# Kernel tuning notes

Measured on AMD Instinct MI355X. Metric: run time of the kernel, lower is better.

## Reference

```python
import jax, jax.numpy as jnp
import numpy as np

B, T, W, F, H = 4, 1024, 33, 512, 8
DK = F // H


def setup_inputs() -> dict:
    key = jax.random.key(0)
    ks = jax.random.split(key, 12)
    s = 1.0 / np.sqrt(F)
    return {
        "query": jax.random.normal(ks[0], (B, T, F), jnp.float32),
        "key": jax.random.normal(ks[1], (B, T, W, F), jnp.float32),
        "value": jax.random.normal(ks[2], (B, T, W, F), jnp.float32),
        "mask": jnp.ones((B, 1, T, W), jnp.int32),
        "Wq": jax.random.uniform(ks[3], (F, F), jnp.float32, -s, s),
        "bq": jax.random.uniform(ks[4], (F,), jnp.float32, -s, s),
        "Wk": jax.random.uniform(ks[5], (F, F), jnp.float32, -s, s),
        "bk": jax.random.uniform(ks[6], (F,), jnp.float32, -s, s),
        "Wv": jax.random.uniform(ks[7], (F, F), jnp.float32, -s, s),
        "bv": jax.random.uniform(ks[8], (F,), jnp.float32, -s, s),
        "Wo": jax.random.uniform(ks[9], (F, F), jnp.float32, -s, s),
        "bo": jax.random.uniform(ks[10], (F,), jnp.float32, -s, s),
    }


def reference(query, key, value, mask, Wq, bq, Wk, bk, Wv, bv, Wo, bo):
    b, t, w, f = key.shape
    # projections
    q = (query @ Wq + bq).reshape(b, t, H, DK)            # (B,T,H,Dk)
    k = (key @ Wk + bk).reshape(b, t, w, H, DK)           # (B,T,W,H,Dk)
    v = (value @ Wv + bv).reshape(b, t, w, H, DK)
    # windowed scores: each query attends to its own window of keys
    scores = jnp.einsum("bthd,btwhd->bhtw", q, k) / jnp.sqrt(jnp.asarray(DK, q.dtype))
    m = (mask == 0)                                       # (B,1,T,W), broadcasts over heads
    min_value = jnp.finfo(scores.dtype).min
    scores = jnp.where(m, min_value, scores)
    attn = jax.nn.softmax(scores, axis=-1)
    attn = jnp.where(m, 0.0, attn)                        # (B,H,T,W)
    x = jnp.einsum("bhtw,btwhd->bthd", attn, v).reshape(b, t, H * DK)
    return x @ Wo + bo
```

## Files before the change

### kernel.cpp

```cpp
#include <hip/hip_runtime.h>
#include <hip/hip_bf16.h>
#include <cstdint>

#define B_ 4
#define T_ 1024
#define W_ 33
#define F_ 512
#define H_ 8
#define DK_ 64

typedef __attribute__((ext_vector_type(8))) short short8;
typedef __attribute__((ext_vector_type(4))) float f32x4;

__device__ __forceinline__ float b2f(ushort u) {
  return __uint_as_float(((uint32_t)u) << 16);
}
__device__ __forceinline__ ushort f2b(float f) {
  union { __hip_bfloat16 b; ushort u; } cv;
  cv.b = __float2bfloat16(f);
  return cv.u;
}

__global__ void convert_w(const float* __restrict__ Wq, const float* __restrict__ Wk,
                          const float* __restrict__ Wv, const float* __restrict__ Wo,
                          ushort* __restrict__ out)
{
  int which = blockIdx.y;
  const float* src = (which == 0) ? Wq : (which == 1) ? Wk : (which == 2) ? Wv : Wo;
  ushort* dst = out + (size_t)which * 262144;
  int idx = blockIdx.x * 256 + threadIdx.x;
  int e = idx & 7;
  int l = (idx >> 3) & 63;
  float v;
  if (which == 1) {
    int kc  = (idx >> 9) & 1;
    int ntf = (idx >> 10) & 31;
    int h   = idx >> 15;
    v = src[(size_t)(ntf * 16 + (l & 15)) * 512 + h * 64 + kc * 32 + ((l >> 4) << 3) + e];
  } else {
    int kc = (idx >> 9) & 15;
    int nt = idx >> 13;
    int k = kc * 32 + ((l >> 4) << 3) + e;
    int n = (nt << 4) + (l & 15);
    v = src[(size_t)k * 512 + n];
  }
  dst[idx] = f2b(v);
}

template<bool A_F32, bool OUT_F32>
__global__ __launch_bounds__(256, 2)
void gemm_pipe(const void* __restrict__ Ap, const ushort* __restrict__ Bf,
               const float* __restrict__ bias, void* __restrict__ Cp, float scale)
{
  __shared__ ushort lA[3][128 * 64];

  const int tid  = threadIdx.x;
  const int lane = tid & 63;
  const int wid  = tid >> 6;
  const int wr   = wid >> 1, wc = wid & 1;
  const int lrow = lane & 15;
  const int lk8  = (lane >> 4) * 8;

  int nwg  = gridDim.x;
  int xcd  = blockIdx.x & 7;
  int slot = blockIdx.x >> 3;
  int q8   = nwg >> 3, r8 = nwg & 7;
  int base = (xcd < r8) ? xcd * (q8 + 1) : r8 * (q8 + 1) + (xcd - r8) * q8;
  int L    = base + slot;
  int bm   = L >> 2;
  int bn   = L & 3;

  int lb_[4];
  size_t asrc_[4];
#pragma unroll
  for (int p = 0; p < 4; ++p) {
    int c   = p * 256 + tid;
    int row = c >> 3;
    int kc  = (c & 7) * 8;
    lb_[p]  = (row * 128 + kc * 2) ^ ((row & 7) << 4);
    asrc_[p] = (size_t)(bm * 128 + row) * 512 + kc;
  }

  const int ntb = bn * 8 + wc * 4;

  float4 P0a0[4], P0a1[4], P1a0[4], P1a1[4];
  short8 P0r[4], P1r[4];
  short8 Q0[8], Q1[8];

  auto issueA = [&](int ks, float4 (&d0)[4], float4 (&d1)[4], short8 (&dr)[4]) {
#pragma unroll
    for (int p = 0; p < 4; ++p) {
      if (A_F32) {
        const float* src = (const float*)Ap + asrc_[p] + ks * 64;
        d0[p] = *(const float4*)src;
        d1[p] = *(const float4*)(src + 4);
      } else {
        dr[p] = *(const short8*)((const ushort*)Ap + asrc_[p] + ks * 64);
      }
    }
  };
  auto lwriteA = [&](int buf, float4 (&d0)[4], float4 (&d1)[4], short8 (&dr)[4]) {
#pragma unroll
    for (int p = 0; p < 4; ++p) {
      short8 hv;
      if (A_F32) {
        hv[0] = (short)f2b(d0[p].x); hv[1] = (short)f2b(d0[p].y);
        hv[2] = (short)f2b(d0[p].z); hv[3] = (short)f2b(d0[p].w);
        hv[4] = (short)f2b(d1[p].x); hv[5] = (short)f2b(d1[p].y);
        hv[6] = (short)f2b(d1[p].z); hv[7] = (short)f2b(d1[p].w);
      } else {
        hv = dr[p];
      }
      *(short8*)((char*)lA[buf] + lb_[p]) = hv;
    }
  };
  auto loadB = [&](int ks, short8 (&dq)[8]) {
#pragma unroll
    for (int kk = 0; kk < 2; ++kk)
#pragma unroll
      for (int nf = 0; nf < 4; ++nf)
        dq[kk * 4 + nf] = *(const short8*)(Bf +
            (((size_t)(ntb + nf) * 16 + ks * 2 + kk) * 64 + lane) * 8);
  };

  f32x4 acc[4][4];
#pragma unroll
  for (int i = 0; i < 4; ++i)
#pragma unroll
    for (int j = 0; j < 4; ++j) acc[i][j] = {0.f, 0.f, 0.f, 0.f};

  auto computeStep = [&](int buf, short8 (&dq)[8]) {
#pragma unroll
    for (int kk = 0; kk < 2; ++kk) {
      short8 af[4];
#pragma unroll
      for (int mf = 0; mf < 4; ++mf) {
        int row = wr * 64 + mf * 16 + lrow;
        int off = (row * 128 + (kk * 32 + lk8) * 2) ^ ((row & 7) << 4);
        af[mf] = *(const short8*)((const char*)lA[buf] + off);
      }
#pragma unroll
      for (int mf = 0; mf < 4; ++mf)
#pragma unroll
        for (int nf = 0; nf < 4; ++nf)
          acc[mf][nf] = __builtin_amdgcn_mfma_f32_16x16x32_bf16(af[mf], dq[kk * 4 + nf], acc[mf][nf], 0, 0, 0);
    }
  };

  issueA(0, P0a0, P0a1, P0r);
  issueA(1, P1a0, P1a1, P1r);
  loadB(0, Q0);
  lwriteA(0, P0a0, P0a1, P0r);
  __syncthreads();

#define GSTEP(T, PWa0, PWa1, PWr, PIa0, PIa1, PIr, QW, QR)                    \
  {                                                                           \
    if ((T) + 1 < 8) lwriteA(((T) + 1) % 3, PWa0, PWa1, PWr);                 \
    if ((T) + 2 < 8) issueA((T) + 2, PIa0, PIa1, PIr);                        \
    if ((T) + 1 < 8) loadB((T) + 1, QW);                                      \
    computeStep((T) % 3, QR);                                                 \
    if ((T) < 7) __syncthreads();                                             \
  }

  GSTEP(0, P1a0, P1a1, P1r, P0a0, P0a1, P0r, Q1, Q0)
  GSTEP(1, P0a0, P0a1, P0r, P1a0, P1a1, P1r, Q0, Q1)
  GSTEP(2, P1a0, P1a1, P1r, P0a0, P0a1, P0r, Q1, Q0)
  GSTEP(3, P0a0, P0a1, P0r, P1a0, P1a1, P1r, Q0, Q1)
  GSTEP(4, P1a0, P1a1, P1r, P0a0, P0a1, P0r, Q1, Q0)
  GSTEP(5, P0a0, P0a1, P0r, P1a0, P1a1, P1r, Q0, Q1)
  GSTEP(6, P1a0, P1a1, P1r, P0a0, P0a1, P0r, Q1, Q0)
  GSTEP(7, P0a0, P0a1, P0r, P1a0, P1a1, P1r, Q0, Q1)
#undef GSTEP

  float bs[4];
#pragma unroll
  for (int nf = 0; nf < 4; ++nf)
    bs[nf] = bias[bn * 128 + wc * 64 + nf * 16 + lrow];

  const int r0 = (lane >> 4) * 4;
#pragma unroll
  for (int mf = 0; mf < 4; ++mf) {
#pragma unroll
    for (int nf = 0; nf < 4; ++nf) {
      int gcol = bn * 128 + wc * 64 + nf * 16 + lrow;
#pragma unroll
      for (int r = 0; r < 4; ++r) {
        int grow = bm * 128 + wr * 64 + mf * 16 + r0 + r;
        float val = (acc[mf][nf][r] + bs[nf]) * scale;
        if (OUT_F32) ((float*)Cp)[(size_t)grow * 512 + gcol] = val;
        else         ((ushort*)Cp)[(size_t)grow * 512 + gcol] = f2b(val);
      }
    }
  }
}

__global__ __launch_bounds__(256, 4)
void r_gemm(const ushort* __restrict__ q, const ushort* __restrict__ WkR,
            ushort* __restrict__ R)
{
  const int tid  = threadIdx.x;
  const int lane = tid & 63;
  const int wid  = tid >> 6;
  const int lr   = lane & 15;
  const int l8   = (lane >> 4) * 8;
  const int mg   = blockIdx.x >> 1;
  const int nh   = blockIdx.x & 1;
  const int h    = blockIdx.y;
  const int m0   = mg * 64;
  const int ntb  = nh * 16 + wid * 4;

  short8 af[2][4], bg[2][4];
#pragma unroll
  for (int ks = 0; ks < 2; ++ks)
#pragma unroll
    for (int mf = 0; mf < 4; ++mf)
      af[ks][mf] = *(const short8*)(q + (size_t)(m0 + mf * 16 + lr) * 512 + h * 64 + ks * 32 + l8);
#pragma unroll
  for (int ks = 0; ks < 2; ++ks)
#pragma unroll
    for (int nf = 0; nf < 4; ++nf)
      bg[ks][nf] = *(const short8*)(WkR + ((size_t)((h * 32 + ntb + nf) * 2 + ks) * 64 + lane) * 8);

  f32x4 acc[4][4];
#pragma unroll
  for (int i = 0; i < 4; ++i)
#pragma unroll
    for (int j = 0; j < 4; ++j) acc[i][j] = {0.f, 0.f, 0.f, 0.f};

#pragma unroll
  for (int ks = 0; ks < 2; ++ks)
#pragma unroll
    for (int mf = 0; mf < 4; ++mf)
#pragma unroll
      for (int nf = 0; nf < 4; ++nf)
        acc[mf][nf] = __builtin_amdgcn_mfma_f32_16x16x32_bf16(af[ks][mf], bg[ks][nf], acc[mf][nf], 0, 0, 0);

  const int rr = (lane >> 4) * 4;
#pragma unroll
  for (int mf = 0; mf < 4; ++mf)
#pragma unroll
    for (int nf = 0; nf < 4; ++nf) {
      int col = nh * 256 + wid * 64 + nf * 16 + lr;
#pragma unroll
      for (int r = 0; r < 4; ++r) {
        int row = m0 + mf * 16 + rr + r;
        R[((size_t)row * 8 + h) * 512 + col] = f2b(acc[mf][nf][r]);
      }
    }
}

__global__ __launch_bounds__(256, 3)
void attn_fused(const float* __restrict__ key, const float* __restrict__ value,
                const ushort* __restrict__ R, const int* __restrict__ mask,
                ushort* __restrict__ g, float* __restrict__ asum)
{
  __shared__ float sc[H_][W_ + 3];
  __shared__ float lin[H_];
  __shared__ int   msk[W_];

  const int tid  = threadIdx.x;
  const int lane = tid & 63;
  const int wv   = tid >> 6;
  const int bt   = blockIdx.x;

  if (tid < W_) msk[tid] = mask[(size_t)bt * W_ + tid];

  float Rf[8][8];
  {
    const ushort* Rb = R + (size_t)bt * 4096 + lane * 8;
#pragma unroll
    for (int h = 0; h < 8; ++h) {
      short8 rv = *(const short8*)(Rb + h * 512);
#pragma unroll
      for (int j = 0; j < 8; ++j) Rf[h][j] = b2f((ushort)rv[j]);
    }
  }

  const float* kb = key + (size_t)bt * (W_ * 512) + lane * 8;
  for (int w = wv; w < W_; w += 4) {
    float4 k0 = *(const float4*)(kb + (size_t)w * 512);
    float4 k1 = *(const float4*)(kb + (size_t)w * 512 + 4);
    float s[8];
#pragma unroll
    for (int h = 0; h < 8; ++h)
      s[h] = k0.x * Rf[h][0] + k0.y * Rf[h][1] + k0.z * Rf[h][2] + k0.w * Rf[h][3]
           + k1.x * Rf[h][4] + k1.y * Rf[h][5] + k1.z * Rf[h][6] + k1.w * Rf[h][7];
#pragma unroll
    for (int m = 1; m < 64; m <<= 1)
#pragma unroll
      for (int h = 0; h < 8; ++h) s[h] += __shfl_xor(s[h], m, 64);
    if (lane == 0) {
#pragma unroll
      for (int h = 0; h < 8; ++h) sc[h][w] = s[h];
    }
  }
  __syncthreads();

  if (tid < H_) {
    float mx = -3.4028234663852886e38f;
    bool any = false;
    for (int w = 0; w < W_; ++w)
      if (msk[w]) { mx = fmaxf(mx, sc[tid][w]); any = true; }
    float ss = 0.f;
    for (int w = 0; w < W_; ++w) {
      float e = msk[w] ? __expf(sc[tid][w] - mx) : 0.f;
      sc[tid][w] = e;
      ss += e;
    }
    lin[tid] = any ? 1.f / ss : 0.f;
    asum[(size_t)bt * H_ + tid] = any ? 1.f : 0.f;
  }
  __syncthreads();

  const float* vb2 = value + (size_t)bt * (W_ * 512) + tid * 2;
  float g0[8], g1[8];
#pragma unroll
  for (int h = 0; h < 8; ++h) { g0[h] = 0.f; g1[h] = 0.f; }

#pragma unroll
  for (int w = 0; w < W_; ++w) {
    float2 v = *(const float2*)(vb2 + (size_t)w * 512);
#pragma unroll
    for (int h = 0; h < 8; ++h) {
      float a = sc[h][w];
      g0[h] += a * v.x;
      g1[h] += a * v.y;
    }
  }

  ushort* gb = g + (size_t)bt * 4096 + tid * 2;
#pragma unroll
  for (int h = 0; h < 8; ++h) {
    float inv = lin[h];
    ushort2 pk;
    pk.x = f2b(g0[h] * inv);
    pk.y = f2b(g1[h] * inv);
    *(ushort2*)(gb + h * 512) = pk;
  }
}

__global__ __launch_bounds__(256, 2)
void x_proj(const ushort* __restrict__ g, const ushort* __restrict__ WtV,
            const float* __restrict__ bv, const float* __restrict__ asum,
            ushort* __restrict__ x)
{
  const int tid  = threadIdx.x;
  const int lane = tid & 63;
  const int wid  = tid >> 6;
  const int lr   = lane & 15;
  const int l8   = (lane >> 4) * 8;
  const int h    = blockIdx.y;
  const int m0   = blockIdx.x * 256 + wid * 64;
  const int ntb  = h * 4;

  f32x4 acc[4][4];
#pragma unroll
  for (int i = 0; i < 4; ++i)
#pragma unroll
    for (int j = 0; j < 4; ++j) acc[i][j] = {0.f, 0.f, 0.f, 0.f};

  short8 a0[4], a1[4], b0[4], b1[4];

  auto issue = [&](int ks, short8 (&A)[4], short8 (&Bq)[4]) {
#pragma unroll
    for (int mf = 0; mf < 4; ++mf)
      A[mf] = *(const short8*)(g + ((size_t)(m0 + mf * 16 + lr) * 8 + h) * 512 + ks * 32 + l8);
#pragma unroll
    for (int nf = 0; nf < 4; ++nf)
      Bq[nf] = *(const short8*)(WtV + ((size_t)((ntb + nf) * 16 + ks) * 64 + lane) * 8);
  };
  auto step = [&](short8 (&A)[4], short8 (&Bq)[4]) {
#pragma unroll
    for (int mf = 0; mf < 4; ++mf)
#pragma unroll
      for (int nf = 0; nf < 4; ++nf)
        acc[mf][nf] = __builtin_amdgcn_mfma_f32_16x16x32_bf16(A[mf], Bq[nf], acc[mf][nf], 0, 0, 0);
  };

  issue(0, a0, b0);
  issue(1, a1, b1);
#pragma unroll 1
  for (int ks = 0; ks < 16; ks += 2) {
    step(a0, b0);
    if (ks + 2 < 16) issue(ks + 2, a0, b0);
    step(a1, b1);
    if (ks + 3 < 16) issue(ks + 3, a1, b1);
  }

  float bvv[4];
#pragma unroll
  for (int nf = 0; nf < 4; ++nf)
    bvv[nf] = bv[h * 64 + nf * 16 + lr];

  const int rr = (lane >> 4) * 4;
#pragma unroll
  for (int mf = 0; mf < 4; ++mf)
#pragma unroll
    for (int nf = 0; nf < 4; ++nf) {
      int col = h * 64 + nf * 16 + lr;
#pragma unroll
      for (int r = 0; r < 4; ++r) {
        int row = m0 + mf * 16 + rr + r;
        float val = acc[mf][nf][r] + asum[(size_t)row * 8 + h] * bvv[nf];
        x[(size_t)row * 512 + col] = f2b(val);
      }
    }
}

extern "C" void kernel_launch(void* const* d_in, const int* in_sizes, int n_in,
                              void* d_out, int out_size, void* d_ws, size_t ws_size,
                              hipStream_t stream)
{
  const float* query = (const float*)d_in[0];
  const float* key   = (const float*)d_in[1];
  const float* value = (const float*)d_in[2];
  const int*   mask  = (const int*)d_in[3];
  const float* Wq    = (const float*)d_in[4];
  const float* bq    = (const float*)d_in[5];
  const float* Wk    = (const float*)d_in[6];
  const float* bk    = (const float*)d_in[7];
  const float* Wv    = (const float*)d_in[8];
  const float* bv    = (const float*)d_in[9];
  const float* Wo    = (const float*)d_in[10];
  const float* bo    = (const float*)d_in[11];
  (void)bk;

  char* ws = (char*)d_ws;
  ushort* Wt   = (ushort*)ws;
  ushort* WtQ  = Wt;
  ushort* WkR  = Wt + 262144;
  ushort* WtV  = Wt + 524288;
  ushort* WtO  = Wt + 786432;
  ushort* qws  = (ushort*)(ws + (size_t)2  * 1024 * 1024);
  ushort* Rws  = (ushort*)(ws + (size_t)6  * 1024 * 1024);
  ushort* gws  = (ushort*)(ws + (size_t)38 * 1024 * 1024);
  float*  asum = (float*) (ws + (size_t)70 * 1024 * 1024);
  ushort* xws  = (ushort*)(ws + (size_t)71 * 1024 * 1024);

  convert_w<<<dim3(1024, 4), 256, 0, stream>>>(Wq, Wk, Wv, Wo, Wt);

  gemm_pipe<true, false><<<dim3(128, 1), 256, 0, stream>>>(query, WtQ, bq, qws, 0.125f);

  r_gemm<<<dim3(128, 8), 256, 0, stream>>>(qws, WkR, Rws);

  attn_fused<<<dim3(B_ * T_, 1), 256, 0, stream>>>(key, value, Rws, mask, gws, asum);

  x_proj<<<dim3(16, 8), 256, 0, stream>>>(gws, WtV, bv, asum, xws);

  gemm_pipe<false, true><<<dim3(128, 1), 256, 0, stream>>>(xws, WtO, bo, d_out, 1.0f);
}
```

Measured before the change: 193.3 us.

## Assign one wavefront per query position in windowed attention kernel

Each wavefront now handles one (b,t) position instead of one block per position. This removes block-wide __syncthreads and the serial 8-thread softmax. The score reduction uses a transpose-style select-and-shuffle so each lane ends up holding one head's sum. The mask is kept as a ballot bitmask, and value accumulation uses 8 columns per lane across all heads with wide bf16 stores. The cost is many more registers per thread (64 accumulators plus 64 R values), which may lower occupancy, and each wave now streams all 33 key and value rows serially.

```diff
diff --git a/kernel.cpp b/kernel.cpp
--- a/kernel.cpp
+++ b/kernel.cpp
@@ -249,21 +249,22 @@
     }
 }
 
-__global__ __launch_bounds__(256, 3)
+__global__ __launch_bounds__(256)
 void attn_fused(const float* __restrict__ key, const float* __restrict__ value,
                 const ushort* __restrict__ R, const int* __restrict__ mask,
                 ushort* __restrict__ g, float* __restrict__ asum)
 {
-  __shared__ float sc[H_][W_ + 3];
-  __shared__ float lin[H_];
-  __shared__ int   msk[W_];
+  __shared__ float lsc[4][8][36];
+  __shared__ float linv[4][8];
 
   const int tid  = threadIdx.x;
   const int lane = tid & 63;
   const int wv   = tid >> 6;
-  const int bt   = blockIdx.x;
-
-  if (tid < W_) msk[tid] = mask[(size_t)bt * W_ + tid];
+  const int bt   = blockIdx.x * 4 + wv;
+
+  int mreg = 0;
+  if (lane < W_) mreg = mask[(size_t)bt * W_ + lane];
+  unsigned long long mbits = __ballot(mreg != 0);
 
   float Rf[8][8];
   {
@@ -277,7 +278,8 @@
   }
 
   const float* kb = key + (size_t)bt * (W_ * 512) + lane * 8;
-  for (int w = wv; w < W_; w += 4) {
+#pragma unroll 2
+  for (int w = 0; w < W_; ++w) {
     float4 k0 = *(const float4*)(kb + (size_t)w * 512);
     float4 k1 = *(const float4*)(kb + (size_t)w * 512 + 4);
     float s[8];
@@ -286,56 +288,69 @@
       s[h] = k0.x * Rf[h][0] + k0.y * Rf[h][1] + k0.z * Rf[h][2] + k0.w * Rf[h][3]
            + k1.x * Rf[h][4] + k1.y * Rf[h][5] + k1.z * Rf[h][6] + k1.w * Rf[h][7];
 #pragma unroll
-    for (int m = 1; m < 64; m <<= 1)
+    for (int m = 1; m <= 4; m <<= 1)
 #pragma unroll
       for (int h = 0; h < 8; ++h) s[h] += __shfl_xor(s[h], m, 64);
-    if (lane == 0) {
-#pragma unroll
-      for (int h = 0; h < 8; ++h) sc[h][w] = s[h];
-    }
-  }
-  __syncthreads();
-
-  if (tid < H_) {
-    float mx = -3.4028234663852886e38f;
-    bool any = false;
-    for (int w = 0; w < W_; ++w)
-      if (msk[w]) { mx = fmaxf(mx, sc[tid][w]); any = true; }
-    float ss = 0.f;
-    for (int w = 0; w < W_; ++w) {
-      float e = msk[w] ? __expf(sc[tid][w] - mx) : 0.f;
-      sc[tid][w] = e;
-      ss += e;
-    }
-    lin[tid] = any ? 1.f / ss : 0.f;
-    asum[(size_t)bt * H_ + tid] = any ? 1.f : 0.f;
-  }
-  __syncthreads();
-
-  const float* vb2 = value + (size_t)bt * (W_ * 512) + tid * 2;
-  float g0[8], g1[8];
-#pragma unroll
-  for (int h = 0; h < 8; ++h) { g0[h] = 0.f; g1[h] = 0.f; }
-
-#pragma unroll
+    float ta = (lane & 1) ? s[1] : s[0];
+    float tb = (lane & 1) ? s[3] : s[2];
+    float tc = (lane & 1) ? s[5] : s[4];
+    float td = (lane & 1) ? s[7] : s[6];
+    float ua = (lane & 2) ? tb : ta;
+    float ub = (lane & 2) ? td : tc;
+    float t  = (lane & 4) ? ub : ua;
+    t += __shfl_xor(t, 8, 64);
+    t += __shfl_xor(t, 16, 64);
+    t += __shfl_xor(t, 32, 64);
+    t = ((mbits >> w) & 1ull) ? t : -3.0e38f;
+    if (lane < 8) lsc[wv][lane][w] = t;
+  }
+
+  const int hh = lane & 7;
+  float mx = -3.4028234663852886e38f;
+  for (int w = 0; w < W_; ++w) mx = fmaxf(mx, lsc[wv][hh][w]);
+  float ss = 0.f;
   for (int w = 0; w < W_; ++w) {
-    float2 v = *(const float2*)(vb2 + (size_t)w * 512);
+    float e = ((mbits >> w) & 1ull) ? __expf(lsc[wv][hh][w] - mx) : 0.f;
+    ss += e;
+    if (lane < 8) lsc[wv][lane][w] = e;
+  }
+  float inv = (ss > 0.5f) ? 1.f / ss : 0.f;
+  if (lane < 8) {
+    linv[wv][lane] = inv;
+    asum[(size_t)bt * H_ + lane] = (mbits != 0ull) ? 1.f : 0.f;
+  }
+
+  float gg[8][8];
+#pragma unroll
+  for (int h = 0; h < 8; ++h)
+#pragma unroll
+    for (int c = 0; c < 8; ++c) gg[h][c] = 0.f;
+
+  const float* vb = value + (size_t)bt * (W_ * 512) + lane * 8;
+#pragma unroll 2
+  for (int w = 0; w < W_; ++w) {
+    float4 v0 = *(const float4*)(vb + (size_t)w * 512);
+    float4 v1 = *(const float4*)(vb + (size_t)w * 512 + 4);
+    float a[8];
+#pragma unroll
+    for (int h = 0; h < 8; ++h) a[h] = lsc[wv][h][w];
 #pragma unroll
     for (int h = 0; h < 8; ++h) {
-      float a = sc[h][w];
-      g0[h] += a * v.x;
-      g1[h] += a * v.y;
-    }
-  }
-
-  ushort* gb = g + (size_t)bt * 4096 + tid * 2;
+      gg[h][0] += a[h] * v0.x; gg[h][1] += a[h] * v0.y;
+      gg[h][2] += a[h] * v0.z; gg[h][3] += a[h] * v0.w;
+      gg[h][4] += a[h] * v1.x; gg[h][5] += a[h] * v1.y;
+      gg[h][6] += a[h] * v1.z; gg[h][7] += a[h] * v1.w;
+    }
+  }
+
+  ushort* gb = g + (size_t)bt * 4096 + lane * 8;
 #pragma unroll
   for (int h = 0; h < 8; ++h) {
-    float inv = lin[h];
-    ushort2 pk;
-    pk.x = f2b(g0[h] * inv);
-    pk.y = f2b(g1[h] * inv);
-    *(ushort2*)(gb + h * 512) = pk;
+    float iv = linv[wv][h];
+    short8 o;
+#pragma unroll
+    for (int c = 0; c < 8; ++c) o[c] = (short)f2b(gg[h][c] * iv);
+    *(short8*)(gb + h * 512) = o;
   }
 }
 
@@ -443,7 +458,7 @@
 
   r_gemm<<<dim3(128, 8), 256, 0, stream>>>(qws, WkR, Rws);
 
-  attn_fused<<<dim3(B_ * T_, 1), 256, 0, stream>>>(key, value, Rws, mask, gws, asum);
+  attn_fused<<<dim3(B_ * T_ / 4, 1), 256, 0, stream>>>(key, value, Rws, mask, gws, asum);
 
   x_proj<<<dim3(16, 8), 256, 0, stream>>>(gws, WtV, bv, asum, xws);
 
```

Measured after the change: 208.5 us. 1.08x slower.

## Prefetch K/V rows into registers and parallelize score reduction and softmax

Applied to the files above, without the earlier changes.

In attn_fused, all key rows a wave needs are loaded into registers before any dot products, and value rows are prefetched in batches before the softmax so global loads overlap with compute. The per-row 64-lane shuffle reduction for 8 heads is replaced by a partial butterfly plus a lane-select transpose, which cuts shuffle count. The mask becomes a wave ballot bitmask, and the softmax exponentials are spread over all threads instead of 8. The extra register arrays raise register pressure, so the launch bound drops from 3 to 2 blocks per CU, trading occupancy for more memory-level parallelism.

```diff
diff --git a/kernel.cpp b/kernel.cpp
--- a/kernel.cpp
+++ b/kernel.cpp
@@ -249,21 +249,23 @@
     }
 }
 
-__global__ __launch_bounds__(256, 3)
+__global__ __launch_bounds__(256, 2)
 void attn_fused(const float* __restrict__ key, const float* __restrict__ value,
                 const ushort* __restrict__ R, const int* __restrict__ mask,
                 ushort* __restrict__ g, float* __restrict__ asum)
 {
   __shared__ float sc[H_][W_ + 3];
-  __shared__ float lin[H_];
-  __shared__ int   msk[W_];
+  __shared__ float la[H_][W_ + 3];
+  __shared__ float linv[H_];
 
   const int tid  = threadIdx.x;
   const int lane = tid & 63;
   const int wv   = tid >> 6;
   const int bt   = blockIdx.x;
 
-  if (tid < W_) msk[tid] = mask[(size_t)bt * W_ + tid];
+  int mreg = 0;
+  if (lane < W_) mreg = mask[(size_t)bt * W_ + lane];
+  unsigned long long mbits = __ballot(mreg != 0);
 
   float Rf[8][8];
   {
@@ -277,64 +279,124 @@
   }
 
   const float* kb = key + (size_t)bt * (W_ * 512) + lane * 8;
-  for (int w = wv; w < W_; w += 4) {
-    float4 k0 = *(const float4*)(kb + (size_t)w * 512);
-    float4 k1 = *(const float4*)(kb + (size_t)w * 512 + 4);
+  float kA[4][8], kB[5][8];
+#pragma unroll
+  for (int jj = 0; jj < 4; ++jj) {
+    int w = wv + jj * 4;
+    float4 a = *(const float4*)(kb + (size_t)w * 512);
+    float4 b = *(const float4*)(kb + (size_t)w * 512 + 4);
+    kA[jj][0] = a.x; kA[jj][1] = a.y; kA[jj][2] = a.z; kA[jj][3] = a.w;
+    kA[jj][4] = b.x; kA[jj][5] = b.y; kA[jj][6] = b.z; kA[jj][7] = b.w;
+  }
+#pragma unroll
+  for (int jj = 0; jj < 4; ++jj) {
+    int w = wv + 16 + jj * 4;
+    float4 a = *(const float4*)(kb + (size_t)w * 512);
+    float4 b = *(const float4*)(kb + (size_t)w * 512 + 4);
+    kB[jj][0] = a.x; kB[jj][1] = a.y; kB[jj][2] = a.z; kB[jj][3] = a.w;
+    kB[jj][4] = b.x; kB[jj][5] = b.y; kB[jj][6] = b.z; kB[jj][7] = b.w;
+  }
+  if (wv == 0) {
+    float4 a = *(const float4*)(kb + (size_t)32 * 512);
+    float4 b = *(const float4*)(kb + (size_t)32 * 512 + 4);
+    kB[4][0] = a.x; kB[4][1] = a.y; kB[4][2] = a.z; kB[4][3] = a.w;
+    kB[4][4] = b.x; kB[4][5] = b.y; kB[4][6] = b.z; kB[4][7] = b.w;
+  }
+
+  auto scoreRow = [&](const float (&kr)[8], int w) {
     float s[8];
 #pragma unroll
     for (int h = 0; h < 8; ++h)
-      s[h] = k0.x * Rf[h][0] + k0.y * Rf[h][1] + k0.z * Rf[h][2] + k0.w * Rf[h][3]
-           + k1.x * Rf[h][4] + k1.y * Rf[h][5] + k1.z * Rf[h][6] + k1.w * Rf[h][7];
-#pragma unroll
-    for (int m = 1; m < 64; m <<= 1)
+      s[h] = kr[0] * Rf[h][0] + kr[1] * Rf[h][1] + kr[2] * Rf[h][2] + kr[3] * Rf[h][3]
+           + kr[4] * Rf[h][4] + kr[5] * Rf[h][5] + kr[6] * Rf[h][6] + kr[7] * Rf[h][7];
+#pragma unroll
+    for (int m = 1; m <= 4; m <<= 1)
 #pragma unroll
       for (int h = 0; h < 8; ++h) s[h] += __shfl_xor(s[h], m, 64);
-    if (lane == 0) {
-#pragma unroll
-      for (int h = 0; h < 8; ++h) sc[h][w] = s[h];
-    }
-  }
+    float ta = (lane & 1) ? s[1] : s[0];
+    float tb = (lane & 1) ? s[3] : s[2];
+    float tc = (lane & 1) ? s[5] : s[4];
+    float td = (lane & 1) ? s[7] : s[6];
+    float ua = (lane & 2) ? tb : ta;
+    float ub = (lane & 2) ? td : tc;
+    float t  = (lane & 4) ? ub : ua;
+    t += __shfl_xor(t, 8, 64);
+    t += __shfl_xor(t, 16, 64);
+    t += __shfl_xor(t, 32, 64);
+    t = ((mbits >> w) & 1ull) ? t : -3.0e38f;
+    if (lane < 8) sc[lane][w] = t;
+  };
+
+#pragma unroll
+  for (int jj = 0; jj < 4; ++jj) scoreRow(kA[jj], wv + jj * 4);
+#pragma unroll
+  for (int jj = 0; jj < 4; ++jj) scoreRow(kB[jj], wv + 16 + jj * 4);
+  if (wv == 0) scoreRow(kB[4], 32);
   __syncthreads();
 
+  const float* vb = value + (size_t)bt * (W_ * 512) + tid * 2;
+  float2 vA[8], vB[8], vC[8];
+#pragma unroll
+  for (int i = 0; i < 8; ++i) vA[i] = *(const float2*)(vb + (size_t)i * 512);
+#pragma unroll
+  for (int i = 0; i < 8; ++i) vB[i] = *(const float2*)(vb + (size_t)(8 + i) * 512);
+#pragma unroll
+  for (int i = 0; i < 8; ++i) vC[i] = *(const float2*)(vb + (size_t)(16 + i) * 512);
+
+  const int hh = tid & 7;
+  float mx = -3.4028234663852886e38f;
+#pragma unroll
+  for (int w = 0; w < W_; ++w) mx = fmaxf(mx, sc[hh][w]);
+  float ss = 0.f;
+#pragma unroll
+  for (int w = 0; w < W_; ++w)
+    ss += ((mbits >> w) & 1ull) ? __expf(sc[hh][w] - mx) : 0.f;
+
+  for (int t = tid; t < H_ * W_ + (264 - H_ * W_); t += 256) {
+    if (t < 264) {
+      int w = t >> 3;
+      la[hh][w] = ((mbits >> w) & 1ull) ? __expf(sc[hh][w] - mx) : 0.f;
+    }
+  }
   if (tid < H_) {
-    float mx = -3.4028234663852886e38f;
-    bool any = false;
-    for (int w = 0; w < W_; ++w)
-      if (msk[w]) { mx = fmaxf(mx, sc[tid][w]); any = true; }
-    float ss = 0.f;
-    for (int w = 0; w < W_; ++w) {
-      float e = msk[w] ? __expf(sc[tid][w] - mx) : 0.f;
-      sc[tid][w] = e;
-      ss += e;
-    }
-    lin[tid] = any ? 1.f / ss : 0.f;
-    asum[(size_t)bt * H_ + tid] = any ? 1.f : 0.f;
+    linv[tid] = (ss > 0.5f) ? 1.f / ss : 0.f;
+    asum[(size_t)bt * H_ + tid] = (mbits != 0ull) ? 1.f : 0.f;
   }
   __syncthreads();
 
-  const float* vb2 = value + (size_t)bt * (W_ * 512) + tid * 2;
-  float g0[8], g1[8];
-#pragma unroll
-  for (int h = 0; h < 8; ++h) { g0[h] = 0.f; g1[h] = 0.f; }
-
-#pragma unroll
-  for (int w = 0; w < W_; ++w) {
-    float2 v = *(const float2*)(vb2 + (size_t)w * 512);
+  float gg0[8], gg1[8];
+#pragma unroll
+  for (int h = 0; h < 8; ++h) { gg0[h] = 0.f; gg1[h] = 0.f; }
+
+  auto consume = [&](float2 v, int w) {
 #pragma unroll
     for (int h = 0; h < 8; ++h) {
-      float a = sc[h][w];
-      g0[h] += a * v.x;
-      g1[h] += a * v.y;
-    }
-  }
+      float a = la[h][w];
+      gg0[h] += a * v.x;
+      gg1[h] += a * v.y;
+    }
+  };
+
+#pragma unroll
+  for (int i = 0; i < 8; ++i) consume(vA[i], i);
+#pragma unroll
+  for (int i = 0; i < 8; ++i) vA[i] = *(const float2*)(vb + (size_t)(24 + i) * 512);
+#pragma unroll
+  for (int i = 0; i < 8; ++i) consume(vB[i], 8 + i);
+  float2 vL = *(const float2*)(vb + (size_t)32 * 512);
+#pragma unroll
+  for (int i = 0; i < 8; ++i) consume(vC[i], 16 + i);
+#pragma unroll
+  for (int i = 0; i < 8; ++i) consume(vA[i], 24 + i);
+  consume(vL, 32);
 
   ushort* gb = g + (size_t)bt * 4096 + tid * 2;
 #pragma unroll
   for (int h = 0; h < 8; ++h) {
-    float inv = lin[h];
+    float iv = linv[h];
     ushort2 pk;
-    pk.x = f2b(g0[h] * inv);
-    pk.y = f2b(g1[h] * inv);
+    pk.x = f2b(gg0[h] * iv);
+    pk.y = f2b(gg1[h] * iv);
     *(ushort2*)(gb + h * 512) = pk;
   }
 }
```

Measured after the change: 180.3 us. -6.7%, faster.
